# Performance work log

Hardware: AMD Instinct MI355X
Metric: run time of the kernel (lower is better)

Reference implementation:

```python
import jax, jax.numpy as jnp
import numpy as np

MAXDISP = 48
NUM_GROUPS = 40
CONCAT_CH = 12
BN_EPS = 1e-5


def conv3d(x, w):
    # x: [B,C,D,H,W], w: [O,I,3,3,3], stride 1, pad 1
    return jax.lax.conv_general_dilated(
        x, w, window_strides=(1, 1, 1), padding=[(1, 1), (1, 1), (1, 1)],
        dimension_numbers=('NCDHW', 'OIDHW', 'NCDHW'))


def bn_relu(x, gamma, beta, mean, var):
    # inference-style BatchNorm3d followed by ReLU
    inv = gamma * jax.lax.rsqrt(var + BN_EPS)
    sh = (1, -1, 1, 1, 1)
    return jax.nn.relu(x * inv.reshape(sh) + (beta - mean * inv).reshape(sh))


def build_volume(lg, rg, lc, rc):
    # Fused gwc + concat volume: for disparity d, valid region is columns [d:].
    # Columns [:d] are zero (matches the torch new_zeros + sliced writes).
    B, Cg, H, W = lg.shape
    cpg = Cg // NUM_GROUPS
    slices = []
    for d in range(MAXDISP):  # fixed structural loop over disparities
        if d == 0:
            l, r, lcc, rcc = lg, rg, lc, rc
        else:
            l = lg[:, :, :, d:]
            r = rg[:, :, :, :W - d]
            lcc = lc[:, :, :, d:]
            rcc = rc[:, :, :, :W - d]
        corr = (l * r).reshape(B, NUM_GROUPS, cpg, H, W - d).mean(axis=2)
        s = jnp.concatenate([corr, lcc, rcc], axis=1)  # [B, G+2Cc, H, W-d]
        if d > 0:
            s = jnp.pad(s, ((0, 0), (0, 0), (0, 0), (d, 0)))
        slices.append(s)
    return jnp.stack(slices, axis=2)  # [B, G+2Cc, D, H, W]


def setup_inputs() -> dict:
    key = jax.random.key(0)
    ks = jax.random.split(key, 10)
    B, H, W = 4, 64, 128
    Cin = NUM_GROUPS + 2 * CONCAT_CH  # 64
    f32 = jnp.float32
    return {
        'left_gwc': jax.random.normal(ks[0], (B, 320, H, W), f32),
        'right_gwc': jax.random.normal(ks[1], (B, 320, H, W), f32),
        'left_concat': jax.random.normal(ks[2], (B, CONCAT_CH, H, W), f32),
        'right_concat': jax.random.normal(ks[3], (B, CONCAT_CH, H, W), f32),
        'w1': jax.random.normal(ks[4], (32, Cin, 3, 3, 3), f32) * 0.05,
        'g1': jnp.ones((32,), f32),
        'b1': jnp.zeros((32,), f32),
        'm1': jnp.zeros((32,), f32),
        'v1': jnp.ones((32,), f32),
        'w2': jax.random.normal(ks[5], (32, 32, 3, 3, 3), f32) * 0.05,
        'g2': jnp.ones((32,), f32),
        'b2': jnp.zeros((32,), f32),
        'm2': jnp.zeros((32,), f32),
        'v2': jnp.ones((32,), f32),
    }


def reference(left_gwc, right_gwc, left_concat, right_concat,
              w1, g1, b1, m1, v1, w2, g2, b2, m2, v2):
    vol = build_volume(left_gwc, right_gwc, left_concat, right_concat)
    x = bn_relu(conv3d(vol, w1), g1, b1, m1, v1)
    x = bn_relu(conv3d(x, w2), g2, b2, m2, v2)
    return x  # [B, 32, D, H, W]
```

## Files before the change

kernel.cpp:

```cpp
#include <hip/hip_runtime.h>
#include <cstdint>
#include <cstddef>

typedef unsigned short u16;
typedef __bf16 bf16x8 __attribute__((ext_vector_type(8)));
typedef float f32x4 __attribute__((ext_vector_type(4)));

#define MAXDISP 48
#define HH 64
#define WW 128

__device__ __forceinline__ float bf2f(unsigned int x) {
    union { unsigned int i; float f; } c; c.i = x << 16; return c.f;
}
__device__ __forceinline__ float bf2f_hi(unsigned int x) {
    union { unsigned int i; float f; } c; c.i = x & 0xffff0000u; return c.f;
}
__device__ __forceinline__ u16 f2bf(float f) {
    union { float f; unsigned int i; } c; c.f = f;
    unsigned int x = c.i;
    return (u16)((x + 0x7fffu + ((x >> 16) & 1u)) >> 16);
}

__global__ __launch_bounds__(256) void wfrag_kernel(
    const float* __restrict__ w, const float* __restrict__ gam,
    const float* __restrict__ bet, const float* __restrict__ mea,
    const float* __restrict__ var,
    u16* __restrict__ dst, float* __restrict__ bias, int CIN, int KC)
{
    int idx = blockIdx.x * 256 + threadIdx.x;
    int n = 9 * 2 * KC * 512;
    if (idx < n) {
        int j    = idx & 7;
        int lane = (idx >> 3) & 63;
        int t2   = idx >> 9;
        int kc   = t2 % KC;
        int t3   = t2 / KC;
        int nt   = t3 & 1;
        int tap  = t3 >> 1;
        int co   = nt * 16 + (lane & 15);
        int qq   = lane >> 4;
        int kw, c;
        if (CIN == 64) { kw = kc >> 1; c = (kc & 1) * 32 + qq * 8 + j; }
        else           { kw = kc;      c = qq * 8 + j; }
        int kd = tap / 3, kh = tap % 3;
        float inv = gam[co] * rsqrtf(var[co] + 1e-5f);
        dst[idx] = f2bf(w[((size_t)co * CIN + c) * 27 + kd * 9 + kh * 3 + kw] * inv);
    }
    if (blockIdx.x == 0 && threadIdx.x < 32) {
        int co = threadIdx.x;
        float inv = gam[co] * rsqrtf(var[co] + 1e-5f);
        bias[co] = bet[co] - mea[co] * inv;
    }
}

#define RS 334
__global__ __launch_bounds__(256) void vol_build_kernel(
    const float* __restrict__ lg, const float* __restrict__ rg,
    const float* __restrict__ lc, const float* __restrict__ rc,
    u16* __restrict__ vol, int b0)
{
    __shared__ u16 r_s[128 * RS];
    __shared__ u16 o_s[4 * 128 * 68];

    int bi  = blockIdx.x;
    int h   = bi & 63;
    int dh  = (bi >> 6) & 1;
    int bl  = bi >> 7;
    int b   = b0 + bl;
    int tid = threadIdx.x;
    int w    = tid & 127;
    int part = tid >> 7;

    for (int idx = tid; idx < 320 * 32; idx += 256) {
        int c = idx >> 5, w4 = (idx & 31) << 2;
        const float4 v = *(const float4*)(rg + (((size_t)b * 320 + c) * 64 + h) * 128 + w4);
        r_s[(w4 + 0) * RS + c] = f2bf(v.x);
        r_s[(w4 + 1) * RS + c] = f2bf(v.y);
        r_s[(w4 + 2) * RS + c] = f2bf(v.z);
        r_s[(w4 + 3) * RS + c] = f2bf(v.w);
    }
    for (int idx = tid; idx < 12 * 32; idx += 256) {
        int c = idx >> 5, w4 = (idx & 31) << 2;
        const float4 v = *(const float4*)(rc + (((size_t)b * 12 + c) * 64 + h) * 128 + w4);
        r_s[(w4 + 0) * RS + 320 + c] = f2bf(v.x);
        r_s[(w4 + 1) * RS + 320 + c] = f2bf(v.y);
        r_s[(w4 + 2) * RS + 320 + c] = f2bf(v.z);
        r_s[(w4 + 3) * RS + 320 + c] = f2bf(v.w);
    }
    u16 lcv[12];
    if (part == 0) {
#pragma unroll
        for (int k = 0; k < 12; k++)
            lcv[k] = f2bf(lc[(((size_t)b * 12 + k) * 64 + h) * 128 + w]);
    }
    __syncthreads();

    int d0 = dh * 24;
    for (int dc = 0; dc < 24; dc += 4) {
        for (int gb = 0; gb < 5; gb++) {
            int g0 = part * 20 + gb * 4;
            float lv[4][8];
#pragma unroll
            for (int gg = 0; gg < 4; gg++)
#pragma unroll
                for (int j = 0; j < 8; j++)
                    lv[gg][j] = lg[(((size_t)b * 320 + (g0 + gg) * 8 + j) * 64 + h) * 128 + w];
#pragma unroll
            for (int dl = 0; dl < 4; dl++) {
                int d = d0 + dc + dl;
                union { u16 us[4]; uint2 u2; } pk;
                pk.us[0] = pk.us[1] = pk.us[2] = pk.us[3] = 0;
                if (w >= d) {
#pragma unroll
                    for (int gg = 0; gg < 4; gg++) {
                        float s = 0.f;
                        int base = (w - d) * RS + (g0 + gg) * 8;
#pragma unroll
                        for (int jj = 0; jj < 4; jj++) {
                            unsigned int uu = *(const unsigned int*)&r_s[base + jj * 2];
                            s += lv[gg][jj * 2]     * bf2f(uu & 0xffffu);
                            s += lv[gg][jj * 2 + 1] * bf2f_hi(uu);
                        }
                        pk.us[gg] = f2bf(s * 0.125f);
                    }
                }
                *(uint2*)&o_s[(dl * 128 + w) * 68 + g0] = pk.u2;
            }
        }
#pragma unroll
        for (int dl = 0; dl < 4; dl++) {
            int d = d0 + dc + dl;
            union { u16 us[12]; uint2 u2[3]; } z;
            if (part == 0) {
#pragma unroll
                for (int k = 0; k < 12; k++) z.us[k] = (w >= d) ? lcv[k] : (u16)0;
                u16* dst = &o_s[(dl * 128 + w) * 68 + 40];
                *(uint2*)(dst + 0) = z.u2[0];
                *(uint2*)(dst + 4) = z.u2[1];
                *(uint2*)(dst + 8) = z.u2[2];
            } else {
                if (w >= d) {
                    int base = (w - d) * RS + 320;
#pragma unroll
                    for (int k = 0; k < 12; k++) z.us[k] = r_s[base + k];
                } else {
#pragma unroll
                    for (int k = 0; k < 12; k++) z.us[k] = 0;
                }
                u16* dst = &o_s[(dl * 128 + w) * 68 + 52];
                *(uint2*)(dst + 0) = z.u2[0];
                *(uint2*)(dst + 4) = z.u2[1];
                *(uint2*)(dst + 8) = z.u2[2];
            }
        }
        __syncthreads();
#pragma unroll
        for (int i = 0; i < 16; i++) {
            int idx = i * 256 + tid;
            int dl  = idx >> 10;
            int rem = idx & 1023;
            int ww  = rem >> 3, cg = rem & 7;
            const u16* sp = &o_s[(dl * 128 + ww) * 68 + cg * 8];
            uint2 lo = *(const uint2*)sp;
            uint2 hi = *(const uint2*)(sp + 4);
            uint4 ov = { lo.x, lo.y, hi.x, hi.y };
            int d = d0 + dc + dl;
            *(uint4*)(vol + ((((size_t)bl * 48 + d) * 64 + h) * 128 + ww) * 64 + cg * 8) = ov;
        }
        __syncthreads();
    }
}

__global__ __launch_bounds__(256) void conv1_mfma_kernel(
    const u16* __restrict__ vol, const u16* __restrict__ wf,
    const float* __restrict__ bias, u16* __restrict__ x1)
{
    __shared__ u16 a_s[1170 * 8];

    int p  = blockIdx.x;
    int bi = (p & 7) * 768 + (p >> 3);
    int h  = bi & 63;
    int t1 = bi >> 6;
    int d  = t1 % 48;
    int bl = t1 / 48;
    int tid  = threadIdx.x;
    int lane = tid & 63, wid = tid >> 6;
    int lm = lane & 15, q = lane >> 4;

    f32x4 acc[2][2];
#pragma unroll
    for (int i = 0; i < 2; i++)
#pragma unroll
        for (int j = 0; j < 2; j++) acc[i][j] = { 0.f, 0.f, 0.f, 0.f };

    for (int kd = 0; kd < 3; kd++) {
        int dd = d + kd - 1;
        if (dd < 0 || dd >= 48) continue;
        for (int kh = 0; kh < 3; kh++) {
            int hh = h + kh - 1;
            if (hh < 0 || hh >= 64) continue;
            int tap = kd * 3 + kh;

            __syncthreads();
            const u16* src = vol + (((size_t)bl * 48 + dd) * 64 + hh) * 8192;
#pragma unroll
            for (int i = 0; i < 4; i++) {
                int idx = i * 256 + tid;
                int wp = (idx >> 3) + 1, cg = idx & 7;
                uint4 v = *(const uint4*)(src + idx * 8);
                *(uint4*)&a_s[(wp * 9 + cg) * 8] = v;
            }
            if (tid < 16) {
                uint4 z = { 0, 0, 0, 0 };
                int wp = (tid >> 3) ? 129 : 0;
                *(uint4*)&a_s[(wp * 9 + (tid & 7)) * 8] = z;
            }
            __syncthreads();

            bf16x8 bfr[2][6];
#pragma unroll
            for (int nt = 0; nt < 2; nt++)
#pragma unroll
                for (int kc = 0; kc < 6; kc++)
                    bfr[nt][kc] = *(const bf16x8*)(wf + (((size_t)tap * 2 + nt) * 6 + kc) * 512 + lane * 8);

#pragma unroll
            for (int kc = 0; kc < 6; kc++) {
                int kw = kc >> 1;
                int cg = (kc & 1) * 4 + q;
#pragma unroll
                for (int mt = 0; mt < 2; mt++) {
                    int wp = (wid * 2 + mt) * 16 + lm + kw;
                    bf16x8 afr = *(const bf16x8*)&a_s[(wp * 9 + cg) * 8];
                    acc[mt][0] = __builtin_amdgcn_mfma_f32_16x16x32_bf16(afr, bfr[0][kc], acc[mt][0], 0, 0, 0);
                    acc[mt][1] = __builtin_amdgcn_mfma_f32_16x16x32_bf16(afr, bfr[1][kc], acc[mt][1], 0, 0, 0);
                }
            }
        }
    }

    u16* xb = x1 + (((size_t)bl * 48 + d) * 64 + h) * 4096;
#pragma unroll
    for (int mt = 0; mt < 2; mt++)
#pragma unroll
        for (int nt = 0; nt < 2; nt++) {
            int co = nt * 16 + lm;
            float bs = bias[co];
#pragma unroll
            for (int r = 0; r < 4; r++) {
                int w = (wid * 2 + mt) * 16 + q * 4 + r;
                xb[w * 32 + co] = f2bf(fmaxf(acc[mt][nt][r] + bs, 0.f));
            }
        }
}

__global__ __launch_bounds__(256) void conv2_mfma_kernel(
    const u16* __restrict__ x1, const u16* __restrict__ wf,
    const float* __restrict__ bias, float* __restrict__ out, int b0)
{
    __shared__ u16 a_s[650 * 8];

    int p  = blockIdx.x;
    int bi = (p & 7) * 768 + (p >> 3);
    int h  = bi & 63;
    int t1 = bi >> 6;
    int d  = t1 % 48;
    int bl = t1 / 48;
    int tid  = threadIdx.x;
    int lane = tid & 63, wid = tid >> 6;
    int lm = lane & 15, q = lane >> 4;

    f32x4 acc[2][2];
#pragma unroll
    for (int i = 0; i < 2; i++)
#pragma unroll
        for (int j = 0; j < 2; j++) acc[i][j] = { 0.f, 0.f, 0.f, 0.f };

    for (int kd = 0; kd < 3; kd++) {
        int dd = d + kd - 1;
        if (dd < 0 || dd >= 48) continue;
        for (int kh = 0; kh < 3; kh++) {
            int hh = h + kh - 1;
            if (hh < 0 || hh >= 64) continue;
            int tap = kd * 3 + kh;

            __syncthreads();
            const u16* src = x1 + (((size_t)bl * 48 + dd) * 64 + hh) * 4096;
#pragma unroll
            for (int i = 0; i < 2; i++) {
                int idx = i * 256 + tid;
                int wp = (idx >> 2) + 1, cg = idx & 3;
                uint4 v = *(const uint4*)(src + idx * 8);
                *(uint4*)&a_s[(wp * 5 + cg) * 8] = v;
            }
            if (tid < 8) {
                uint4 z = { 0, 0, 0, 0 };
                int wp = (tid >> 2) ? 129 : 0;
                *(uint4*)&a_s[(wp * 5 + (tid & 3)) * 8] = z;
            }
            __syncthreads();

            bf16x8 bfr[2][3];
#pragma unroll
            for (int nt = 0; nt < 2; nt++)
#pragma unroll
                for (int kc = 0; kc < 3; kc++)
                    bfr[nt][kc] = *(const bf16x8*)(wf + (((size_t)tap * 2 + nt) * 3 + kc) * 512 + lane * 8);

#pragma unroll
            for (int kc = 0; kc < 3; kc++) {
                int kw = kc;
#pragma unroll
                for (int mt = 0; mt < 2; mt++) {
                    int wp = (wid * 2 + mt) * 16 + lm + kw;
                    bf16x8 afr = *(const bf16x8*)&a_s[(wp * 5 + q) * 8];
                    acc[mt][0] = __builtin_amdgcn_mfma_f32_16x16x32_bf16(afr, bfr[0][kc], acc[mt][0], 0, 0, 0);
                    acc[mt][1] = __builtin_amdgcn_mfma_f32_16x16x32_bf16(afr, bfr[1][kc], acc[mt][1], 0, 0, 0);
                }
            }
        }
    }

#pragma unroll
    for (int mt = 0; mt < 2; mt++)
#pragma unroll
        for (int nt = 0; nt < 2; nt++) {
            int co = nt * 16 + lm;
            float bs = bias[co];
            float4 o;
            o.x = fmaxf(acc[mt][nt][0] + bs, 0.f);
            o.y = fmaxf(acc[mt][nt][1] + bs, 0.f);
            o.z = fmaxf(acc[mt][nt][2] + bs, 0.f);
            o.w = fmaxf(acc[mt][nt][3] + bs, 0.f);
            int wbase = (wid * 2 + mt) * 16 + q * 4;
            *(float4*)(out + ((((size_t)(b0 + bl) * 32 + co) * 48 + d) * 64 + h) * 128 + wbase) = o;
        }
}

extern "C" void kernel_launch(void* const* d_in, const int* in_sizes, int n_in,
                              void* d_out, int out_size, void* d_ws, size_t ws_size,
                              hipStream_t stream)
{
    const float* lg = (const float*)d_in[0];
    const float* rg = (const float*)d_in[1];
    const float* lc = (const float*)d_in[2];
    const float* rc = (const float*)d_in[3];
    const float* w1 = (const float*)d_in[4];
    const float* g1 = (const float*)d_in[5];
    const float* b1 = (const float*)d_in[6];
    const float* m1 = (const float*)d_in[7];
    const float* v1 = (const float*)d_in[8];
    const float* w2 = (const float*)d_in[9];
    const float* g2 = (const float*)d_in[10];
    const float* b2 = (const float*)d_in[11];
    const float* m2 = (const float*)d_in[12];
    const float* v2 = (const float*)d_in[13];
    (void)in_sizes; (void)n_in; (void)out_size; (void)ws_size;

    char* ws = (char*)d_ws;
    u16*   wf1   = (u16*)ws;
    u16*   wf2   = (u16*)(ws + 110592);
    float* bias1 = (float*)(ws + 165888);
    float* bias2 = (float*)(ws + 166016);
    u16*   x1    = (u16*)(ws + 166144);

    wfrag_kernel<<<216, 256, 0, stream>>>(w1, g1, b1, m1, v1, wf1, bias1, 64, 6);
    wfrag_kernel<<<108, 256, 0, stream>>>(w2, g2, b2, m2, v2, wf2, bias2, 32, 3);

    for (int r = 0; r < 2; r++) {
        u16* vol = (u16*)d_out + (size_t)r * 50331648;
        vol_build_kernel<<<256, 256, 0, stream>>>(lg, rg, lc, rc, vol, 2 * r);
        conv1_mfma_kernel<<<6144, 256, 0, stream>>>(vol, wf1, bias1, x1);
        conv2_mfma_kernel<<<6144, 256, 0, stream>>>(x1, wf2, bias2, (float*)d_out, 2 * r);
    }
}
```

Baseline: 725.1 us.

## Prefetch next conv tap plane into registers to overlap global loads with MFMA

Both conv kernels now load the next (kd,kh) input plane into registers while the current tap's MFMAs run. Clamped plane indices replace the early-continue skips, so the loop fully unrolls with a uniform barrier structure, and taps that fall outside the volume skip only the compute. The zero halo columns in shared memory are written once at kernel start instead of every tap. The cost is extra registers for the staging buffer and redundant loads of clamped planes at the volume edges.

```diff
diff --git a/kernel.cpp b/kernel.cpp
--- a/kernel.cpp
+++ b/kernel.cpp
@@ -188,59 +188,78 @@
     int lane = tid & 63, wid = tid >> 6;
     int lm = lane & 15, q = lane >> 4;
 
+    if (tid < 16) {
+        uint4 z = { 0, 0, 0, 0 };
+        int wp = (tid >> 3) ? 129 : 0;
+        *(uint4*)&a_s[(wp * 9 + (tid & 7)) * 8] = z;
+    }
+
     f32x4 acc[2][2];
 #pragma unroll
     for (int i = 0; i < 2; i++)
 #pragma unroll
         for (int j = 0; j < 2; j++) acc[i][j] = { 0.f, 0.f, 0.f, 0.f };
 
+    const size_t blb = (size_t)bl * 48;
+#define C1_PLANE(kd_, kh_) \
+    (vol + (((blb + (size_t)min(max(d + (kd_) - 1, 0), 47)) * 64 + min(max(h + (kh_) - 1, 0), 63))) * 8192)
+
+    uint4 st[4];
+    {
+        const u16* src = C1_PLANE(0, 0);
+#pragma unroll
+        for (int i = 0; i < 4; i++) st[i] = *(const uint4*)(src + (i * 256 + tid) * 8);
+    }
+
+#pragma unroll
     for (int kd = 0; kd < 3; kd++) {
-        int dd = d + kd - 1;
-        if (dd < 0 || dd >= 48) continue;
+#pragma unroll
         for (int kh = 0; kh < 3; kh++) {
-            int hh = h + kh - 1;
-            if (hh < 0 || hh >= 64) continue;
             int tap = kd * 3 + kh;
 
             __syncthreads();
-            const u16* src = vol + (((size_t)bl * 48 + dd) * 64 + hh) * 8192;
 #pragma unroll
             for (int i = 0; i < 4; i++) {
                 int idx = i * 256 + tid;
-                int wp = (idx >> 3) + 1, cg = idx & 7;
-                uint4 v = *(const uint4*)(src + idx * 8);
-                *(uint4*)&a_s[(wp * 9 + cg) * 8] = v;
-            }
-            if (tid < 16) {
-                uint4 z = { 0, 0, 0, 0 };
-                int wp = (tid >> 3) ? 129 : 0;
-                *(uint4*)&a_s[(wp * 9 + (tid & 7)) * 8] = z;
+                *(uint4*)&a_s[(((idx >> 3) + 1) * 9 + (idx & 7)) * 8] = st[i];
             }
             __syncthreads();
 
-            bf16x8 bfr[2][6];
-#pragma unroll
-            for (int nt = 0; nt < 2; nt++)
-#pragma unroll
-                for (int kc = 0; kc < 6; kc++)
-                    bfr[nt][kc] = *(const bf16x8*)(wf + (((size_t)tap * 2 + nt) * 6 + kc) * 512 + lane * 8);
-
-#pragma unroll
-            for (int kc = 0; kc < 6; kc++) {
-                int kw = kc >> 1;
-                int cg = (kc & 1) * 4 + q;
-#pragma unroll
-                for (int mt = 0; mt < 2; mt++) {
-                    int wp = (wid * 2 + mt) * 16 + lm + kw;
-                    bf16x8 afr = *(const bf16x8*)&a_s[(wp * 9 + cg) * 8];
-                    acc[mt][0] = __builtin_amdgcn_mfma_f32_16x16x32_bf16(afr, bfr[0][kc], acc[mt][0], 0, 0, 0);
-                    acc[mt][1] = __builtin_amdgcn_mfma_f32_16x16x32_bf16(afr, bfr[1][kc], acc[mt][1], 0, 0, 0);
+            if (tap < 8) {
+                int nkd = (tap + 1) / 3, nkh = (tap + 1) % 3;
+                const u16* src = C1_PLANE(nkd, nkh);
+#pragma unroll
+                for (int i = 0; i < 4; i++) st[i] = *(const uint4*)(src + (i * 256 + tid) * 8);
+            }
+
+            bool valid = (kd == 0 ? (d > 0) : (kd == 2 ? (d < 47) : true))
+                      && (kh == 0 ? (h > 0) : (kh == 2 ? (h < 63) : true));
+            if (valid) {
+                bf16x8 bfr[2][6];
+#pragma unroll
+                for (int nt = 0; nt < 2; nt++)
+#pragma unroll
+                    for (int kc = 0; kc < 6; kc++)
+                        bfr[nt][kc] = *(const bf16x8*)(wf + (((size_t)tap * 2 + nt) * 6 + kc) * 512 + lane * 8);
+
+#pragma unroll
+                for (int kc = 0; kc < 6; kc++) {
+                    int kw = kc >> 1;
+                    int cg = (kc & 1) * 4 + q;
+#pragma unroll
+                    for (int mt = 0; mt < 2; mt++) {
+                        int wp = (wid * 2 + mt) * 16 + lm + kw;
+                        bf16x8 afr = *(const bf16x8*)&a_s[(wp * 9 + cg) * 8];
+                        acc[mt][0] = __builtin_amdgcn_mfma_f32_16x16x32_bf16(afr, bfr[0][kc], acc[mt][0], 0, 0, 0);
+                        acc[mt][1] = __builtin_amdgcn_mfma_f32_16x16x32_bf16(afr, bfr[1][kc], acc[mt][1], 0, 0, 0);
+                    }
                 }
             }
         }
     }
-
-    u16* xb = x1 + (((size_t)bl * 48 + d) * 64 + h) * 4096;
+#undef C1_PLANE
+
+    u16* xb = x1 + ((blb + d) * 64 + h) * 4096;
 #pragma unroll
     for (int mt = 0; mt < 2; mt++)
 #pragma unroll
@@ -271,56 +290,75 @@
     int lane = tid & 63, wid = tid >> 6;
     int lm = lane & 15, q = lane >> 4;
 
+    if (tid < 8) {
+        uint4 z = { 0, 0, 0, 0 };
+        int wp = (tid >> 2) ? 129 : 0;
+        *(uint4*)&a_s[(wp * 5 + (tid & 3)) * 8] = z;
+    }
+
     f32x4 acc[2][2];
 #pragma unroll
     for (int i = 0; i < 2; i++)
 #pragma unroll
         for (int j = 0; j < 2; j++) acc[i][j] = { 0.f, 0.f, 0.f, 0.f };
 
+    const size_t blb = (size_t)bl * 48;
+#define C2_PLANE(kd_, kh_) \
+    (x1 + (((blb + (size_t)min(max(d + (kd_) - 1, 0), 47)) * 64 + min(max(h + (kh_) - 1, 0), 63))) * 4096)
+
+    uint4 st[2];
+    {
+        const u16* src = C2_PLANE(0, 0);
+#pragma unroll
+        for (int i = 0; i < 2; i++) st[i] = *(const uint4*)(src + (i * 256 + tid) * 8);
+    }
+
+#pragma unroll
     for (int kd = 0; kd < 3; kd++) {
-        int dd = d + kd - 1;
-        if (dd < 0 || dd >= 48) continue;
+#pragma unroll
         for (int kh = 0; kh < 3; kh++) {
-            int hh = h + kh - 1;
-            if (hh < 0 || hh >= 64) continue;
             int tap = kd * 3 + kh;
 
             __syncthreads();
-            const u16* src = x1 + (((size_t)bl * 48 + dd) * 64 + hh) * 4096;
 #pragma unroll
             for (int i = 0; i < 2; i++) {
                 int idx = i * 256 + tid;
-                int wp = (idx >> 2) + 1, cg = idx & 3;
-                uint4 v = *(const uint4*)(src + idx * 8);
-                *(uint4*)&a_s[(wp * 5 + cg) * 8] = v;
-            }
-            if (tid < 8) {
-                uint4 z = { 0, 0, 0, 0 };
-                int wp = (tid >> 2) ? 129 : 0;
-                *(uint4*)&a_s[(wp * 5 + (tid & 3)) * 8] = z;
+                *(uint4*)&a_s[(((idx >> 2) + 1) * 5 + (idx & 3)) * 8] = st[i];
             }
             __syncthreads();
 
-            bf16x8 bfr[2][3];
-#pragma unroll
-            for (int nt = 0; nt < 2; nt++)
-#pragma unroll
-                for (int kc = 0; kc < 3; kc++)
-                    bfr[nt][kc] = *(const bf16x8*)(wf + (((size_t)tap * 2 + nt) * 3 + kc) * 512 + lane * 8);
-
-#pragma unroll
-            for (int kc = 0; kc < 3; kc++) {
-                int kw = kc;
-#pragma unroll
-                for (int mt = 0; mt < 2; mt++) {
-                    int wp = (wid * 2 + mt) * 16 + lm + kw;
-                    bf16x8 afr = *(const bf16x8*)&a_s[(wp * 5 + q) * 8];
-                    acc[mt][0] = __builtin_amdgcn_mfma_f32_16x16x32_bf16(afr, bfr[0][kc], acc[mt][0], 0, 0, 0);
-                    acc[mt][1] = __builtin_amdgcn_mfma_f32_16x16x32_bf16(afr, bfr[1][kc], acc[mt][1], 0, 0, 0);
+            if (tap < 8) {
+                int nkd = (tap + 1) / 3, nkh = (tap + 1) % 3;
+                const u16* src = C2_PLANE(nkd, nkh);
+#pragma unroll
+                for (int i = 0; i < 2; i++) st[i] = *(const uint4*)(src + (i * 256 + tid) * 8);
+            }
+
+            bool valid = (kd == 0 ? (d > 0) : (kd == 2 ? (d < 47) : true))
+                      && (kh == 0 ? (h > 0) : (kh == 2 ? (h < 63) : true));
+            if (valid) {
+                bf16x8 bfr[2][3];
+#pragma unroll
+                for (int nt = 0; nt < 2; nt++)
+#pragma unroll
+                    for (int kc = 0; kc < 3; kc++)
+                        bfr[nt][kc] = *(const bf16x8*)(wf + (((size_t)tap * 2 + nt) * 3 + kc) * 512 + lane * 8);
+
+#pragma unroll
+                for (int kc = 0; kc < 3; kc++) {
+                    int kw = kc;
+#pragma unroll
+                    for (int mt = 0; mt < 2; mt++) {
+                        int wp = (wid * 2 + mt) * 16 + lm + kw;
+                        bf16x8 afr = *(const bf16x8*)&a_s[(wp * 5 + q) * 8];
+                        acc[mt][0] = __builtin_amdgcn_mfma_f32_16x16x32_bf16(afr, bfr[0][kc], acc[mt][0], 0, 0, 0);
+                        acc[mt][1] = __builtin_amdgcn_mfma_f32_16x16x32_bf16(afr, bfr[1][kc], acc[mt][1], 0, 0, 0);
+                    }
                 }
             }
         }
     }
+#undef C2_PLANE
 
 #pragma unroll
     for (int mt = 0; mt < 2; mt++)
```

After: 1.162 ms. 1.6x slower.
